# Performance work log

Measured on AMD Instinct MI355X. Metric: run time of the kernel, lower is better.

Reference implementation:

```python
import jax, jax.numpy as jnp
import numpy as np

# Enformer/Borzoi-style MHA with relative positional bias
B, T, C = 2, 1536, 1536          # batch, seq bins, input channels
H, K, V = 8, 64, 192             # heads, key_size, value_size
F = 32                           # num_position_features (borzoi, asymmetric: 2 * 16 basis)


def setup_inputs() -> dict:
    key = jax.random.key(0)
    ks = jax.random.split(key, 9)
    he = lambda fan_in: (2.0 / fan_in) ** 0.5  # he_normal scale
    return {
        "x": jax.random.normal(ks[0], (B, T, C), jnp.float32),
        "Wq": jax.random.normal(ks[1], (C, H * K), jnp.float32) * he(C),
        "Wk": jax.random.normal(ks[2], (C, H * K), jnp.float32) * he(C),
        "Wv": jax.random.normal(ks[3], (C, H * V), jnp.float32) * he(C),
        "Wr": jax.random.normal(ks[4], (F, H * K), jnp.float32) * he(F),
        "r_w_bias": jax.random.normal(ks[5], (1, H, 1, K), jnp.float32) * 0.02,
        "r_r_bias": jax.random.normal(ks[6], (1, H, 1, K), jnp.float32) * 0.02,
        "Wo": jax.random.normal(ks[7], (H * V, H * V), jnp.float32) * he(H * V),
        "bo": jnp.zeros((H * V,), jnp.float32),
    }


def positional_features(positions):
    """Borzoi central-mask basis, absolute=True, asymmetric -> [L, F]."""
    nb = F // 2
    pow_rate = np.exp(np.log(T + 1) / nb).astype(np.float32)
    center_widths = pow_rate ** jnp.arange(1, nb + 1, dtype=jnp.float32) - 1.0  # [nb]
    sign = jnp.sign(positions)
    abs_pos = jnp.abs(positions)
    emb = (center_widths[None, :] > abs_pos[:, None]).astype(jnp.float32)  # [L, nb]
    return jnp.concatenate([emb, sign[:, None] * emb], axis=-1)  # [L, 2*nb]


def relative_shift(x):
    """[B,H,T,2T-1] -> [B,H,T,T] relative-shift trick (pad, reshape, slice)."""
    b, h, t, l = x.shape
    x = jnp.pad(x, ((0, 0), (0, 0), (0, 0), (1, 0)))      # [b,h,t,l+1]
    x = x.reshape(b, h, l + 1, t)[:, :, 1:, :]             # [b,h,l,t]
    x = x.reshape(b, h, t, l)
    return x[..., :t]


def reference(x, Wq, Wk, Wv, Wr, r_w_bias, r_r_bias, Wo, bo):
    q = (x @ Wq).reshape(B, T, H, K).transpose(0, 2, 1, 3)   # [B,H,T,K]
    k = (x @ Wk).reshape(B, T, H, K).transpose(0, 2, 1, 3)
    v = (x @ Wv).reshape(B, T, H, V).transpose(0, 2, 1, 3)   # [B,H,T,V]
    q = q * (K ** -0.5)  # scaling=True

    distances = jnp.arange(-T + 1, T, dtype=jnp.float32)     # [2T-1]
    pe = positional_features(distances)                       # [2T-1, F]
    rk = (pe @ Wr).reshape(2 * T - 1, H, K)                   # [2T-1, H, K]

    content_logits = jnp.einsum('bhtk,bhsk->bhts', q + r_w_bias, k)   # [B,H,T,T]
    rel_logits = jnp.einsum('bhtk,rhk->bhtr', q + r_r_bias, rk)       # [B,H,T,2T-1]
    logits = content_logits + relative_shift(rel_logits)

    weights = jax.nn.softmax(logits, axis=-1)
    out = jnp.einsum('bhts,bhsv->bhtv', weights, v)          # [B,H,T,V]
    out = out.transpose(0, 2, 1, 3).reshape(B, T, H * V)     # [B,T,H*V]
    return out @ Wo + bo
```

## Files before the change

### kernel.cpp

```cpp
#include <hip/hip_runtime.h>
#include <hip/hip_bf16.h>

typedef __hip_bfloat16 bf16;
typedef unsigned short ushort;
typedef unsigned int uint;
typedef __attribute__((ext_vector_type(8))) short short8;
typedef __attribute__((ext_vector_type(4))) float f32x4;

#define Bsz 2
#define Tn  1536
#define Cn  1536
#define Hn  8
#define Kn  64
#define Vn  192

__device__ __forceinline__ ushort f2bs(float f) {
  union { bf16 h; ushort u; } cv;
  cv.h = __float2bfloat16(f);
  return cv.u;
}
__device__ __forceinline__ float bs2f(ushort u) {
  union { float f; uint v; } cv; cv.v = ((uint)u) << 16; return cv.f;
}

__device__ __forceinline__ void gld_lds16(const ushort* g, ushort* l) {
  __builtin_amdgcn_global_load_lds(
      (const __attribute__((address_space(1))) uint*)g,
      (__attribute__((address_space(3))) uint*)l, 16, 0, 0);
}

#define DPP_MAXSTEP(x, ctrl)                                                  \
  do {                                                                        \
    union { float f; int i; } a_, b_;                                         \
    a_.f = (x);                                                               \
    b_.i = __builtin_amdgcn_update_dpp(a_.i, a_.i, (ctrl), 0xf, 0xf, true);   \
    (x) = fmaxf((x), b_.f);                                                   \
  } while (0)

__global__ __launch_bounds__(256) void prep(
    const float* __restrict__ x,  const float* __restrict__ Wq,
    const float* __restrict__ Wk, const float* __restrict__ Wv,
    const float* __restrict__ Wo, const float* __restrict__ Wr,
    ushort* __restrict__ xb, ushort* __restrict__ Wt,
    ushort* __restrict__ Wot, ushort* __restrict__ rkdb,
    unsigned char* __restrict__ lutb) {
  const int z = blockIdx.z;
  if (z < 4) {
    if (z < 2 && blockIdx.x >= 16) return;
    const float* in = (z == 0) ? Wq : (z == 1) ? Wk : (z == 2) ? Wv : Wo;
    ushort* out = (z == 0) ? Wt : (z == 1) ? Wt + 512 * 1536
                : (z == 2) ? Wt + 1024 * 1536 : Wot;
    const int Cc = (z < 2) ? 512 : 1536;
    __shared__ float tile[32][33];
    const int bx = blockIdx.x * 32;
    const int by = blockIdx.y * 32;
    const int tx = threadIdx.x & 31, ty = threadIdx.x >> 5;
#pragma unroll
    for (int i = 0; i < 32; i += 8)
      tile[ty + i][tx] = in[(size_t)(by + ty + i) * Cc + bx + tx];
    __syncthreads();
#pragma unroll
    for (int i = 0; i < 32; i += 8)
      out[(size_t)(bx + ty + i) * 1536 + by + tx] = f2bs(tile[tx][ty + i]);
  } else if (z == 4) {
    const int n4 = 3072 * 1536 / 4;
    for (int i = (blockIdx.y * 48 + blockIdx.x) * 256 + threadIdx.x; i < n4;
         i += 2304 * 256) {
      float4 v = ((const float4*)x)[i];
      uint2 o;
      o.x = (uint)f2bs(v.x) | ((uint)f2bs(v.y) << 16);
      o.y = (uint)f2bs(v.z) | ((uint)f2bs(v.w) << 16);
      ((uint2*)xb)[i] = o;
    }
  } else {
    const int base = (blockIdx.y * 48 + blockIdx.x) * 256 + threadIdx.x;
    if (base < 8 * 40 * 64) {
      const int h = base / 2560, rem = base % 2560, u = rem >> 6, k = rem & 63;
      float acc = 0.f;
      if (u < 33) {
        const float sg = (u == 32) ? 0.f : (u < 16 ? 1.f : -1.f);
        const int c = (u == 32) ? 16 : (u < 16 ? u + 1 : u - 15);
#pragma unroll
        for (int i = 0; i < 16; i++)
          if (i >= 16 - c)
            acc += Wr[i * 512 + h * 64 + k] + sg * Wr[(16 + i) * 512 + h * 64 + k];
      }
      rkdb[h * 2560 + u * 64 + k] = f2bs(acc);
    } else if (base < 8 * 40 * 64 + 3072) {
      const int idx = base - 8 * 40 * 64;
      const int d = idx - 1535;
      const float ad = fabsf((float)d);
      int c = 0;
#pragma unroll
      for (int i = 0; i < 16; i++) {
        double cw = exp(log((double)(Tn + 1)) * (double)(i + 1) / 16.0) - 1.0;
        if ((float)cw > ad) c++;
      }
      lutb[idx] = (unsigned char)((d == 0) ? 32 : (d > 0 ? c - 1 : 15 + c));
    }
  }
}

__global__ __launch_bounds__(256) void gemm_qkv(
    const ushort* __restrict__ xb, const ushort* __restrict__ Wt,
    ushort* __restrict__ qb, ushort* __restrict__ kb, ushort* __restrict__ vtb) {
  __shared__ ushort Al[128 * 32];
  __shared__ ushort Bl[128 * 32];
  const int tid = threadIdx.x;
  const int w = tid >> 6, lane = tid & 63, quad = lane >> 4, ln = lane & 15;
  const int Lb = blockIdx.x + 20 * blockIdx.y;
  const int wg = (Lb & 7) * 60 + (Lb >> 3);
  const int bm = (wg % 24) * 128, bn = (wg / 24) * 128;
  const int wm = (w & 1) * 64, wn = (w >> 1) * 64;
  f32x4 acc[4][4];
#pragma unroll
  for (int i = 0; i < 4; i++)
#pragma unroll
    for (int j = 0; j < 4; j++) acc[i][j] = (f32x4){0.f, 0.f, 0.f, 0.f};

  for (int k0 = 0; k0 < 1536; k0 += 32) {
    __syncthreads();
#pragma unroll
    for (int st = 0; st < 2; st++) {
      int idx = tid + st * 256;
      int row = idx >> 2, col = (idx & 3) * 8;
      gld_lds16(xb + (size_t)(bm + row) * 1536 + k0 + col, Al + idx * 8);
      gld_lds16(Wt + (size_t)(bn + row) * 1536 + k0 + col, Bl + idx * 8);
    }
    __syncthreads();
    short8 af[4], bfr[4];
#pragma unroll
    for (int t = 0; t < 4; t++) {
      af[t]  = *(const short8*)(Al + (wm + t * 16 + ln) * 32 + quad * 8);
      bfr[t] = *(const short8*)(Bl + (wn + t * 16 + ln) * 32 + quad * 8);
    }
#pragma unroll
    for (int mt = 0; mt < 4; mt++)
#pragma unroll
      for (int nt = 0; nt < 4; nt++)
        acc[mt][nt] = __builtin_amdgcn_mfma_f32_16x16x32_bf16(
            af[mt], bfr[nt], acc[mt][nt], 0, 0, 0);
  }

  if (bn < 512) {
#pragma unroll
    for (int mt = 0; mt < 4; mt++)
#pragma unroll
      for (int nt = 0; nt < 4; nt++)
#pragma unroll
        for (int r = 0; r < 4; r++) {
          int m = bm + wm + mt * 16 + quad * 4 + r;
          int n = bn + wn + nt * 16 + ln;
          qb[(size_t)m * 512 + n] = f2bs(acc[mt][nt][r] * 0.125f);
        }
  } else if (bn < 1024) {
#pragma unroll
    for (int mt = 0; mt < 4; mt++)
#pragma unroll
      for (int nt = 0; nt < 4; nt++)
#pragma unroll
        for (int r = 0; r < 4; r++) {
          int m = bm + wm + mt * 16 + quad * 4 + r;
          int n = bn - 512 + wn + nt * 16 + ln;
          kb[(size_t)m * 512 + n] = f2bs(acc[mt][nt][r]);
        }
  } else {
#pragma unroll
    for (int mt = 0; mt < 4; mt++)
#pragma unroll
      for (int nt = 0; nt < 4; nt++) {
        int vcol = bn - 1024 + wn + nt * 16 + ln;
        int m0 = bm + wm + mt * 16 + quad * 4;
        uint2 val;
        val.x = (uint)f2bs(acc[mt][nt][0]) | ((uint)f2bs(acc[mt][nt][1]) << 16);
        val.y = (uint)f2bs(acc[mt][nt][2]) | ((uint)f2bs(acc[mt][nt][3]) << 16);
        *(uint2*)(vtb + (size_t)vcol * 3072 + m0) = val;
      }
  }
}

__global__ __launch_bounds__(256) void gemm_out(
    const ushort* __restrict__ att, const ushort* __restrict__ Wot,
    const float* __restrict__ bo, float* __restrict__ out) {
  __shared__ ushort Al[128 * 32];
  __shared__ ushort Bl[128 * 32];
  const int tid = threadIdx.x;
  const int w = tid >> 6, lane = tid & 63, quad = lane >> 4, ln = lane & 15;
  const int Lb = blockIdx.x + 12 * blockIdx.y;
  const int wg = (Lb & 7) * 36 + (Lb >> 3);
  const int bm = (wg % 24) * 128, bn = (wg / 24) * 128;
  const int wm = (w & 1) * 64, wn = (w >> 1) * 64;
  f32x4 acc[4][4];
#pragma unroll
  for (int i = 0; i < 4; i++)
#pragma unroll
    for (int j = 0; j < 4; j++) acc[i][j] = (f32x4){0.f, 0.f, 0.f, 0.f};

  for (int k0 = 0; k0 < 1536; k0 += 32) {
    __syncthreads();
#pragma unroll
    for (int st = 0; st < 2; st++) {
      int idx = tid + st * 256;
      int row = idx >> 2, col = (idx & 3) * 8;
      gld_lds16(att + (size_t)(bm + row) * 1536 + k0 + col, Al + idx * 8);
      gld_lds16(Wot + (size_t)(bn + row) * 1536 + k0 + col, Bl + idx * 8);
    }
    __syncthreads();
    short8 af[4], bfr[4];
#pragma unroll
    for (int t = 0; t < 4; t++) {
      af[t]  = *(const short8*)(Al + (wm + t * 16 + ln) * 32 + quad * 8);
      bfr[t] = *(const short8*)(Bl + (wn + t * 16 + ln) * 32 + quad * 8);
    }
#pragma unroll
    for (int mt = 0; mt < 4; mt++)
#pragma unroll
      for (int nt = 0; nt < 4; nt++)
        acc[mt][nt] = __builtin_amdgcn_mfma_f32_16x16x32_bf16(
            af[mt], bfr[nt], acc[mt][nt], 0, 0, 0);
  }
#pragma unroll
  for (int mt = 0; mt < 4; mt++)
#pragma unroll
    for (int nt = 0; nt < 4; nt++)
#pragma unroll
      for (int r = 0; r < 4; r++) {
        int m = bm + wm + mt * 16 + quad * 4 + r;
        int n = bn + wn + nt * 16 + ln;
        out[(size_t)m * 1536 + n] = acc[mt][nt][r] + bo[n];
      }
}

__global__ __launch_bounds__(256, 3) void attn_mfma(
    const ushort* __restrict__ qb, const ushort* __restrict__ kb,
    const ushort* __restrict__ vtb, const ushort* __restrict__ rkdb,
    const unsigned char* __restrict__ lutb,
    const float* __restrict__ rwb, const float* __restrict__ rrb,
    ushort* __restrict__ op0, ushort* __restrict__ op1,
    float2* __restrict__ mlb) {
  __shared__ __align__(16) char smem[50176];
  ushort* Kl = (ushort*)smem;
  ushort* Vl = (ushort*)(smem + 8192);
  ushort* Dl = (ushort*)(smem + 32768);
  unsigned char* Ll = (unsigned char*)(smem + 37888);

  const int L  = blockIdx.x + 24 * blockIdx.y + 192 * blockIdx.z;
  const int h  = L & 7;
  const int g  = L >> 3;
  const int bsk = g / 24;
  const int b  = bsk >> 1;
  const int sk = bsk & 1;
  const int t0 = (g - bsk * 24) * 64;
  const int bT = b * Tn;
  const int tid = threadIdx.x;
  const int w = tid >> 6, lane = tid & 63, quad = lane >> 4, ln = lane & 15;

  ushort* Pp = (ushort*)(smem + 40960 + w * 2304);

  const int lr  = lane >> 3;
  const int lcx = (lane & 7) ^ lr;

  {
    const int s0 = sk * 768;
#pragma unroll
    for (int i = 0; i < 2; i++) {
      int kc = w * 2 + i, sr = kc * 8 + lr;
      gld_lds16(kb + (size_t)(bT + s0 + sr) * 512 + h * 64 + lcx * 8,
                (ushort*)(smem + kc * 1024) + lane * 8);
    }
#pragma unroll
    for (int i = 0; i < 6; i++) {
      int kc = w * 6 + i, vr = kc * 8 + lr;
      gld_lds16(vtb + (size_t)(h * 192 + vr) * 3072 + bT + s0 + lcx * 8,
                (ushort*)(smem + 8192 + kc * 1024) + lane * 8);
    }
    if (w < 3)
      gld_lds16((const ushort*)(lutb + w * 1024) + lane * 8,
                (ushort*)(smem + 37888 + w * 1024) + lane * 8);
  }

  short8 qw8[2], qr8[2];
  {
    const ushort* qrow = qb + (size_t)(bT + t0 + 16 * w + ln) * 512 + h * 64;
#pragma unroll
    for (int ks = 0; ks < 2; ks++) {
      int k0 = quad * 8 + ks * 32;
#pragma unroll
      for (int e = 0; e < 8; e++) {
        float qv = bs2f(qrow[k0 + e]);
        qw8[ks][e] = (short)f2bs(qv + rwb[h * 64 + k0 + e]);
        qr8[ks][e] = (short)f2bs(qv + rrb[h * 64 + k0 + e]);
      }
    }
  }

  {
    f32x4 Dacc[3];
#pragma unroll
    for (int ut = 0; ut < 3; ut++) {
      Dacc[ut] = (f32x4){0.f, 0.f, 0.f, 0.f};
#pragma unroll
      for (int ks = 0; ks < 2; ks++) {
        int urow = 16 * ut + ln; urow = urow > 39 ? 39 : urow;
        short8 bfr = *(const short8*)(rkdb + h * 2560 + urow * 64 + quad * 8 + ks * 32);
        Dacc[ut] = __builtin_amdgcn_mfma_f32_16x16x32_bf16(qr8[ks], bfr, Dacc[ut], 0, 0, 0);
      }
    }
    const int trow = 16 * w + 4 * quad;
#pragma unroll
    for (int ut = 0; ut < 2; ut++)
#pragma unroll
      for (int r = 0; r < 4; r++)
        Dl[(trow + r) * 40 + 16 * ut + ln] = f2bs(Dacc[ut][r]);
    if (ln == 0) {
#pragma unroll
      for (int r = 0; r < 4; r++)
        Dl[(trow + r) * 40 + 32] = f2bs(Dacc[2][r]);
    }
  }

  f32x4 Oacc[12];
  f32x4 Lacc = (f32x4){0.f, 0.f, 0.f, 0.f};
  float m_i[4];
#pragma unroll
  for (int vt = 0; vt < 12; vt++) Oacc[vt] = (f32x4){0.f, 0.f, 0.f, 0.f};
#pragma unroll
  for (int r = 0; r < 4; r++) m_i[r] = -1e30f;

  short8 ones8;
#pragma unroll
  for (int e = 0; e < 8; e++) ones8[e] = (short)0x3F80;

  __syncthreads();

  const int ibase = sk * 768 - t0 - 16 * w - 4 * quad + ln + 1535;
  const int tl0 = 16 * w + 4 * quad;

  for (int ch = 0; ch < 12; ch++) {
    float dval[4][4];
#pragma unroll
    for (int ct = 0; ct < 4; ct++)
#pragma unroll
      for (int r = 0; r < 4; r++) {
        int idx = ibase + 64 * ch + 16 * ct - r;
        dval[ct][r] = bs2f(Dl[(tl0 + r) * 40 + Ll[idx]]);
      }

    f32x4 Sacc[4];
    __builtin_amdgcn_s_setprio(1);
#pragma unroll
    for (int ct = 0; ct < 4; ct++) {
      Sacc[ct] = (f32x4){0.f, 0.f, 0.f, 0.f};
#pragma unroll
      for (int ks = 0; ks < 2; ks++) {
        short8 bfr = *(const short8*)(
            Kl + (16 * ct + ln) * 64 + ((quad + 4 * ks) ^ (ln & 7)) * 8);
        Sacc[ct] = __builtin_amdgcn_mfma_f32_16x16x32_bf16(qw8[ks], bfr, Sacc[ct], 0, 0, 0);
      }
    }
    __builtin_amdgcn_s_setprio(0);

    float pS[4][4];
#pragma unroll
    for (int ct = 0; ct < 4; ct++)
#pragma unroll
      for (int r = 0; r < 4; r++)
        pS[ct][r] = Sacc[ct][r] + dval[ct][r];

    float mx[4];
#pragma unroll
    for (int r = 0; r < 4; r++) {
      float m2 = fmaxf(fmaxf(pS[0][r], pS[1][r]), fmaxf(pS[2][r], pS[3][r]));
      DPP_MAXSTEP(m2, 0xB1);
      DPP_MAXSTEP(m2, 0x4E);
      DPP_MAXSTEP(m2, 0x124);
      DPP_MAXSTEP(m2, 0x128);
      mx[r] = m2;
    }
    int need = (mx[0] > m_i[0] + 8.f) | (mx[1] > m_i[1] + 8.f) |
               (mx[2] > m_i[2] + 8.f) | (mx[3] > m_i[3] + 8.f);
    if (__any(need)) {
#pragma unroll
      for (int r = 0; r < 4; r++) {
        float mnew = fmaxf(m_i[r], mx[r]);
        float alpha = __expf(m_i[r] - mnew);
        m_i[r] = mnew;
        Lacc[r] *= alpha;
#pragma unroll
        for (int vt = 0; vt < 12; vt++) Oacc[vt][r] *= alpha;
      }
    }
#pragma unroll
    for (int ct = 0; ct < 4; ct++)
#pragma unroll
      for (int r = 0; r < 4; r++)
        pS[ct][r] = __expf(pS[ct][r] - m_i[r]);
#pragma unroll
    for (int ct = 0; ct < 4; ct++)
#pragma unroll
      for (int r = 0; r < 4; r++)
        Pp[(4 * quad + r) * 72 + 16 * ct + ln] = f2bs(pS[ct][r]);
    __asm__ volatile("s_waitcnt lgkmcnt(0)" ::: "memory");
    short8 afr[2];
#pragma unroll
    for (int ks = 0; ks < 2; ks++)
      afr[ks] = *(const short8*)(Pp + ln * 72 + quad * 8 + ks * 32);

    __syncthreads();

    if (ch < 11) {
      const int s0n = sk * 768 + ch * 64 + 64;
#pragma unroll
      for (int i = 0; i < 2; i++) {
        int kc = w * 2 + i, sr = kc * 8 + lr;
        gld_lds16(kb + (size_t)(bT + s0n + sr) * 512 + h * 64 + lcx * 8,
                  (ushort*)(smem + kc * 1024) + lane * 8);
      }
    }

    __builtin_amdgcn_s_setprio(1);
    Lacc = __builtin_amdgcn_mfma_f32_16x16x32_bf16(afr[0], ones8, Lacc, 0, 0, 0);
    Lacc = __builtin_amdgcn_mfma_f32_16x16x32_bf16(afr[1], ones8, Lacc, 0, 0, 0);
#pragma unroll
    for (int vt = 0; vt < 12; vt++) {
#pragma unroll
      for (int ks = 0; ks < 2; ks++) {
        short8 bfr = *(const short8*)(
            Vl + (16 * vt + ln) * 64 + ((quad + 4 * ks) ^ (ln & 7)) * 8);
        Oacc[vt] = __builtin_amdgcn_mfma_f32_16x16x32_bf16(afr[ks], bfr, Oacc[vt], 0, 0, 0);
      }
    }
    __builtin_amdgcn_s_setprio(0);

    __syncthreads();

    if (ch < 11) {
      const int s0n = sk * 768 + ch * 64 + 64;
#pragma unroll
      for (int i = 0; i < 6; i++) {
        int kc = w * 6 + i, vr = kc * 8 + lr;
        gld_lds16(vtb + (size_t)(h * 192 + vr) * 3072 + bT + s0n + lcx * 8,
                  (ushort*)(smem + 8192 + kc * 1024) + lane * 8);
      }
    }
  }

  ushort* op = sk ? op1 : op0;
  float inv[4];
#pragma unroll
  for (int r = 0; r < 4; r++) inv[r] = 1.f / Lacc[r];
#pragma unroll
  for (int vt = 0; vt < 12; vt++)
#pragma unroll
    for (int r = 0; r < 4; r++) {
      int t = t0 + 16 * w + 4 * quad + r;
      op[(size_t)(bT + t) * 1536 + h * 192 + 16 * vt + ln] = f2bs(Oacc[vt][r] * inv[r]);
    }
  if (ln == 0) {
#pragma unroll
    for (int r = 0; r < 4; r++) {
      int t = t0 + 16 * w + 4 * quad + r;
      float2 v; v.x = m_i[r]; v.y = Lacc[r];
      mlb[((sk * 2 + b) * 8 + h) * 1536 + t] = v;
    }
  }
}

__global__ __launch_bounds__(256) void attn_combine(
    const ushort* __restrict__ op0, const ushort* __restrict__ op1,
    const float2* __restrict__ mlb, ushort* __restrict__ att) {
  int g = blockIdx.x * 256 + threadIdx.x;
  int row = g / 384;
  int c4 = (g - row * 384) * 4;
  int b = row >= 1536;
  int t = row - b * 1536;
  int h = c4 / 192;
  float2 ml0 = mlb[((0 + b) * 8 + h) * 1536 + t];
  float2 ml1 = mlb[((2 + b) * 8 + h) * 1536 + t];
  float M = fmaxf(ml0.x, ml1.x);
  float w0 = __expf(ml0.x - M) * ml0.y;
  float w1 = __expf(ml1.x - M) * ml1.y;
  float inv = 1.f / (w0 + w1);
  w0 *= inv; w1 *= inv;
  size_t off = (size_t)row * 1536 + c4;
  uint2 a = *(const uint2*)(op0 + off);
  uint2 c = *(const uint2*)(op1 + off);
  uint2 o;
  float r0 = w0 * bs2f((ushort)(a.x & 0xffff)) + w1 * bs2f((ushort)(c.x & 0xffff));
  float r1 = w0 * bs2f((ushort)(a.x >> 16))    + w1 * bs2f((ushort)(c.x >> 16));
  float r2 = w0 * bs2f((ushort)(a.y & 0xffff)) + w1 * bs2f((ushort)(c.y & 0xffff));
  float r3 = w0 * bs2f((ushort)(a.y >> 16))    + w1 * bs2f((ushort)(c.y >> 16));
  o.x = (uint)f2bs(r0) | ((uint)f2bs(r1) << 16);
  o.y = (uint)f2bs(r2) | ((uint)f2bs(r3) << 16);
  *(uint2*)(att + off) = o;
}

extern "C" void kernel_launch(void* const* d_in, const int* in_sizes, int n_in,
                              void* d_out, int out_size, void* d_ws, size_t ws_size,
                              hipStream_t stream) {
  const float* x   = (const float*)d_in[0];
  const float* Wq  = (const float*)d_in[1];
  const float* Wk  = (const float*)d_in[2];
  const float* Wv  = (const float*)d_in[3];
  const float* Wr  = (const float*)d_in[4];
  const float* rwb = (const float*)d_in[5];
  const float* rrb = (const float*)d_in[6];
  const float* Wo  = (const float*)d_in[7];
  const float* bo  = (const float*)d_in[8];
  float* out = (float*)d_out;

  char* ws = (char*)d_ws;
  ushort* xb  = (ushort*)ws;
  ushort* op1 = (ushort*)ws;
  ushort* att = (ushort*)ws;
  ushort* Wot = (ushort*)(ws + 9437184);
  ushort* Wt  = (ushort*)(ws + 14155776);
  ushort* op0 = (ushort*)(ws + 14155776);
  ushort* qb  = (ushort*)(ws + 23592960);
  ushort* kb  = (ushort*)(ws + 26738688);
  ushort* vtb = (ushort*)(ws + 29884416);
  unsigned char* lutb = (unsigned char*)(ws + 41287680);
  ushort* rkdb = (ushort*)(ws + 41290752);
  float2* mlb = (float2*)(ws + 42467328);

  prep<<<dim3(48, 48, 6), dim3(256), 0, stream>>>(
      x, Wq, Wk, Wv, Wo, Wr, xb, Wt, Wot, rkdb, lutb);
  gemm_qkv<<<dim3(20, 24), dim3(256), 0, stream>>>(xb, Wt, qb, kb, vtb);
  attn_mfma<<<dim3(24, 8, 4), dim3(256), 0, stream>>>(
      qb, kb, vtb, rkdb, lutb, rwb, rrb, op0, op1, mlb);
  attn_combine<<<dim3(4608), dim3(256), 0, stream>>>(op0, op1, mlb, att);
  gemm_out<<<dim3(12, 24), dim3(256), 0, stream>>>(att, Wot, bo, out);
}
```

Measured before the change: 221.2 us.

## Double-buffer QKV and output GEMMs with BK=64 and XOR-swizzled LDS

Both projection GEMMs now stage 64-wide K slices into two LDS buffers, prefetching the next slice while MFMAs consume the current one. This overlaps global-to-LDS copies with compute and halves the number of barriers per K. An XOR swizzle on the LDS column chunk is meant to avoid bank conflicts on the short8 fragment reads. LDS use per block grows fourfold to 64 KB, which may reduce occupancy.

```diff
diff --git a/kernel.cpp b/kernel.cpp
--- a/kernel.cpp
+++ b/kernel.cpp
@@ -101,13 +101,22 @@
   }
 }
 
+#define STAGE64(src, base_row, kk, dst)                                       \
+  _Pragma("unroll")                                                           \
+  for (int i_ = 0; i_ < 4; i_++) {                                            \
+    int kc_ = w * 4 + i_, sr_ = kc_ * 8 + lr;                                 \
+    gld_lds16(src + (size_t)(base_row + sr_) * 1536 + (kk) + lcx * 8,         \
+              dst + kc_ * 512 + lane * 8);                                    \
+  }
+
 __global__ __launch_bounds__(256) void gemm_qkv(
     const ushort* __restrict__ xb, const ushort* __restrict__ Wt,
     ushort* __restrict__ qb, ushort* __restrict__ kb, ushort* __restrict__ vtb) {
-  __shared__ ushort Al[128 * 32];
-  __shared__ ushort Bl[128 * 32];
+  __shared__ ushort Al[2][128 * 64];
+  __shared__ ushort Bl[2][128 * 64];
   const int tid = threadIdx.x;
   const int w = tid >> 6, lane = tid & 63, quad = lane >> 4, ln = lane & 15;
+  const int lr = lane >> 3, lcx = (lane & 7) ^ lr;
   const int Lb = blockIdx.x + 20 * blockIdx.y;
   const int wg = (Lb & 7) * 60 + (Lb >> 3);
   const int bm = (wg % 24) * 128, bn = (wg / 24) * 128;
@@ -118,28 +127,34 @@
 #pragma unroll
     for (int j = 0; j < 4; j++) acc[i][j] = (f32x4){0.f, 0.f, 0.f, 0.f};
 
-  for (int k0 = 0; k0 < 1536; k0 += 32) {
+  STAGE64(xb, bm, 0, Al[0]);
+  STAGE64(Wt, bn, 0, Bl[0]);
+  __syncthreads();
+
+  int cur = 0;
+  for (int k0 = 0; k0 < 1536; k0 += 64) {
+    if (k0 + 64 < 1536) {
+      STAGE64(xb, bm, k0 + 64, Al[cur ^ 1]);
+      STAGE64(Wt, bn, k0 + 64, Bl[cur ^ 1]);
+    }
+#pragma unroll
+    for (int ks = 0; ks < 2; ks++) {
+      short8 af[4], bfr[4];
+#pragma unroll
+      for (int t = 0; t < 4; t++) {
+        int cx = ((quad + 4 * ks) ^ (ln & 7)) * 8;
+        af[t]  = *(const short8*)(Al[cur] + (wm + t * 16 + ln) * 64 + cx);
+        bfr[t] = *(const short8*)(Bl[cur] + (wn + t * 16 + ln) * 64 + cx);
+      }
+#pragma unroll
+      for (int mt = 0; mt < 4; mt++)
+#pragma unroll
+        for (int nt = 0; nt < 4; nt++)
+          acc[mt][nt] = __builtin_amdgcn_mfma_f32_16x16x32_bf16(
+              af[mt], bfr[nt], acc[mt][nt], 0, 0, 0);
+    }
     __syncthreads();
-#pragma unroll
-    for (int st = 0; st < 2; st++) {
-      int idx = tid + st * 256;
-      int row = idx >> 2, col = (idx & 3) * 8;
-      gld_lds16(xb + (size_t)(bm + row) * 1536 + k0 + col, Al + idx * 8);
-      gld_lds16(Wt + (size_t)(bn + row) * 1536 + k0 + col, Bl + idx * 8);
-    }
-    __syncthreads();
-    short8 af[4], bfr[4];
-#pragma unroll
-    for (int t = 0; t < 4; t++) {
-      af[t]  = *(const short8*)(Al + (wm + t * 16 + ln) * 32 + quad * 8);
-      bfr[t] = *(const short8*)(Bl + (wn + t * 16 + ln) * 32 + quad * 8);
-    }
-#pragma unroll
-    for (int mt = 0; mt < 4; mt++)
-#pragma unroll
-      for (int nt = 0; nt < 4; nt++)
-        acc[mt][nt] = __builtin_amdgcn_mfma_f32_16x16x32_bf16(
-            af[mt], bfr[nt], acc[mt][nt], 0, 0, 0);
+    cur ^= 1;
   }
 
   if (bn < 512) {
@@ -182,10 +197,11 @@
 __global__ __launch_bounds__(256) void gemm_out(
     const ushort* __restrict__ att, const ushort* __restrict__ Wot,
     const float* __restrict__ bo, float* __restrict__ out) {
-  __shared__ ushort Al[128 * 32];
-  __shared__ ushort Bl[128 * 32];
+  __shared__ ushort Al[2][128 * 64];
+  __shared__ ushort Bl[2][128 * 64];
   const int tid = threadIdx.x;
   const int w = tid >> 6, lane = tid & 63, quad = lane >> 4, ln = lane & 15;
+  const int lr = lane >> 3, lcx = (lane & 7) ^ lr;
   const int Lb = blockIdx.x + 12 * blockIdx.y;
   const int wg = (Lb & 7) * 36 + (Lb >> 3);
   const int bm = (wg % 24) * 128, bn = (wg / 24) * 128;
@@ -196,28 +212,34 @@
 #pragma unroll
     for (int j = 0; j < 4; j++) acc[i][j] = (f32x4){0.f, 0.f, 0.f, 0.f};
 
-  for (int k0 = 0; k0 < 1536; k0 += 32) {
+  STAGE64(att, bm, 0, Al[0]);
+  STAGE64(Wot, bn, 0, Bl[0]);
+  __syncthreads();
+
+  int cur = 0;
+  for (int k0 = 0; k0 < 1536; k0 += 64) {
+    if (k0 + 64 < 1536) {
+      STAGE64(att, bm, k0 + 64, Al[cur ^ 1]);
+      STAGE64(Wot, bn, k0 + 64, Bl[cur ^ 1]);
+    }
+#pragma unroll
+    for (int ks = 0; ks < 2; ks++) {
+      short8 af[4], bfr[4];
+#pragma unroll
+      for (int t = 0; t < 4; t++) {
+        int cx = ((quad + 4 * ks) ^ (ln & 7)) * 8;
+        af[t]  = *(const short8*)(Al[cur] + (wm + t * 16 + ln) * 64 + cx);
+        bfr[t] = *(const short8*)(Bl[cur] + (wn + t * 16 + ln) * 64 + cx);
+      }
+#pragma unroll
+      for (int mt = 0; mt < 4; mt++)
+#pragma unroll
+        for (int nt = 0; nt < 4; nt++)
+          acc[mt][nt] = __builtin_amdgcn_mfma_f32_16x16x32_bf16(
+              af[mt], bfr[nt], acc[mt][nt], 0, 0, 0);
+    }
     __syncthreads();
-#pragma unroll
-    for (int st = 0; st < 2; st++) {
-      int idx = tid + st * 256;
-      int row = idx >> 2, col = (idx & 3) * 8;
-      gld_lds16(att + (size_t)(bm + row) * 1536 + k0 + col, Al + idx * 8);
-      gld_lds16(Wot + (size_t)(bn + row) * 1536 + k0 + col, Bl + idx * 8);
-    }
-    __syncthreads();
-    short8 af[4], bfr[4];
-#pragma unroll
-    for (int t = 0; t < 4; t++) {
-      af[t]  = *(const short8*)(Al + (wm + t * 16 + ln) * 32 + quad * 8);
-      bfr[t] = *(const short8*)(Bl + (wn + t * 16 + ln) * 32 + quad * 8);
-    }
-#pragma unroll
-    for (int mt = 0; mt < 4; mt++)
-#pragma unroll
-      for (int nt = 0; nt < 4; nt++)
-        acc[mt][nt] = __builtin_amdgcn_mfma_f32_16x16x32_bf16(
-            af[mt], bfr[nt], acc[mt][nt], 0, 0, 0);
+    cur ^= 1;
   }
 #pragma unroll
   for (int mt = 0; mt < 4; mt++)
```

Result: faster. 211.0 us, median of 3 (-4.6%).
